# Kernel optimization log

Hardware: AMD Instinct MI355X
Metric: run time of the kernel (lower is better)

## Reference

```python
import jax, jax.numpy as jnp
import numpy as np

N_CLASSES = 19


def setup_inputs() -> dict:
    key = jax.random.key(0)
    k1, k2 = jax.random.split(key)
    embedding = jax.random.normal(k1, (4, 32, 128, 128), dtype=jnp.float32)
    label = jax.random.randint(k2, (4, 512, 512), 0, N_CLASSES, dtype=jnp.int64)
    return {"embedding": embedding, "label": label}


def _discriminative_loss(embedding, label, n_classes=N_CLASSES):
    N, H, W = label.shape
    C = embedding.shape[1]
    # bilinear upsample embedding to label resolution (F.upsample mode='bilinear')
    emb = jax.image.resize(embedding, (N, C, H, W), method="bilinear")
    HW = H * W
    emb = emb.reshape(N, C, HW).transpose(0, 2, 1)          # (N, HW, C)
    lab = label.reshape(N, HW)                               # (N, HW)

    onehot = jax.nn.one_hot(lab, n_classes, dtype=emb.dtype)  # (N, HW, K)
    count = onehot.sum(1)                                    # (N, K)
    mask = (count > 0).astype(emb.dtype)                     # (N, K)

    # per-class embedding sum and (biased, /(count+1)) mean
    cls_sum = jnp.einsum("npc,npk->nkc", emb, onehot)       # (N, K, C)
    cls_mean = cls_sum / (count[:, :, None] + 1.0)           # (N, K, C)

    # intra-class: per-pixel squared distance to own-class mean, mean over C
    mean_pp = jnp.take_along_axis(cls_mean, lab[:, :, None], axis=1)  # (N, HW, C)
    d2 = jnp.mean((emb - mean_pp) ** 2, axis=-1)             # (N, HW)
    intra_per_cls = jnp.einsum("np,npk->nk", d2, onehot) / (count + 1.0)  # (N, K)
    n_fg = mask[:, 1:].sum(1)                                # (N,)
    l2_intra = (intra_per_cls[:, 1:] * mask[:, 1:]).sum(1) / n_fg  # (N,)

    # inter-class: pairwise mean squared distance between class means
    diff = cls_mean[:, :, None, :] - cls_mean[:, None, :, :]  # (N, K, K, C)
    inter = jnp.mean(diff ** 2, axis=-1)                     # (N, K, K)
    inter = inter * mask[:, None, :] * mask[:, :, None]
    l2_inter = inter[:, 1:, 1:].reshape(N, -1).sum(1) / (n_fg * n_fg)  # (N,)

    return l2_intra - l2_inter


def reference(embedding, label):
    return _discriminative_loss(embedding, label)
```

## Files before the change

kernel.cpp:

```cpp
#include <hip/hip_runtime.h>

#define NIMG 4
#define NCLS 19
#define CCH  32
#define LH   128
#define LW   128
#define HH   512
#define WW   512
#define HWQ  (LH*LW)
#define HWP  (HH*WW)

#define TR 8
#define TC 8
#define NTX (LW/TC)
#define NTILE (256)
#define TCELLS (TR*TC)
#define RW 10
#define RING 100
#define NSLOT 608

__device__ __forceinline__ void taps(int v, int lim, int& i0, float& w0, float& w1) {
    int r = v & 3;
    int b = (v >> 2) + ((r < 2) ? -1 : 0);
    float f = 0.125f + 0.25f * (float)((r + 2) & 3);
    w0 = 1.f - f; w1 = f;
    if (b < 0)           { b = 0;       w0 = 1.f; w1 = 0.f; }
    else if (b >= lim)   { b = lim - 1; w0 = 0.f; w1 = 1.f; }
    i0 = b;
}

__device__ __forceinline__ float ring_fetch(const float* Gn, int i, int Y0, int X0) {
    int p = i / RING, r = i - p * RING;
    int gy = r / RW, gx = r - gy * RW;
    int yy = Y0 - 1 + gy; yy = yy < 0 ? 0 : (yy > LH - 1 ? LH - 1 : yy);
    int xx = X0 - 1 + gx; xx = xx < 0 ? 0 : (xx > LW - 1 ? LW - 1 : xx);
    return Gn[(size_t)p * HWQ + yy * LW + xx];
}

__global__ __launch_bounds__(256) void k_gram(const float* __restrict__ E,
        float* __restrict__ G) {
    int n = blockIdx.y, rp = blockIdx.x;
    int tid = threadIdx.x;
    int x = tid & 127, dy = tid >> 7;
    int y = rp * 2 + dy;
    int yn = (y < LH - 1) ? y + 1 : y;
    int xn = (x < LW - 1) ? x + 1 : x;
    bool fix = ((x & 63) == 63);
    const float* base = E + (size_t)n * CCH * HWQ;
    const float* Ea = base + y * LW + x;
    const float* Eb = base + yn * LW + x;
    const float* Eax = base + y * LW + xn;
    const float* Ebx = base + yn * LW + xn;
    float gs = 0.f, gh = 0.f, gv = 0.f, gda = 0.f;
#pragma unroll 8
    for (int c = 0; c < CCH; c++) {
        float a = Ea[(size_t)c * HWQ];
        float b = Eb[(size_t)c * HWQ];
        float ar = __shfl_down(a, 1);
        float br = __shfl_down(b, 1);
        if (fix) { ar = Eax[(size_t)c * HWQ]; br = Ebx[(size_t)c * HWQ]; }
        gs = fmaf(a, a, gs);
        gh = fmaf(a, ar, gh);
        gv = fmaf(a, b, gv);
        gda = fmaf(a, br, fmaf(ar, b, gda));
    }
    float* Gp = G + (size_t)n * 4 * HWQ + y * LW + x;
    Gp[0] = gs; Gp[HWQ] = gh; Gp[2 * HWQ] = gv; Gp[3 * HWQ] = gda;
}

__global__ __launch_bounds__(256, 4) void k_field(const float* __restrict__ E,
        const int* __restrict__ lab, const float* __restrict__ G,
        float* __restrict__ P_sum, float* __restrict__ P_cnt, float* __restrict__ P_S2) {
    int tile = blockIdx.x, n = blockIdx.y;
    int ty = tile >> 4, tx = tile & 15;
    int Y0 = ty * TR, X0 = tx * TC;
    __shared__ float A[TCELLS * NCLS];
    __shared__ float Gt[4 * RING];
    __shared__ float S2w[4 * NCLS];
    __shared__ float tmpc[NCLS * 8];
    __shared__ __align__(16) float cs_l[NSLOT];
    int tid = threadIdx.x;
    const int* ln = lab + (size_t)n * HWP;
    int h_lo = Y0 * 4 - 2;

    int hA, qA, hB = 0, qB = 0; bool vB;
    int4 LA, LB = make_int4(0, 0, 0, 0);
    {
        int hr = tid / RW, qi = tid - hr * RW;
        hA = h_lo + hr; qA = X0 - 1 + qi;
        int hc = hA < 0 ? 0 : (hA > HH - 1 ? HH - 1 : hA);
        int qc = qA < 0 ? 0 : (qA > LW - 1 ? LW - 1 : qA);
        LA = *(const int4*)(ln + hc * WW + (qc << 2));
    }
    vB = (tid < 360 - 256);
    if (vB) {
        int i = tid + 256;
        int hr = i / RW, qi = i - hr * RW;
        hB = h_lo + hr; qB = X0 - 1 + qi;
        int hc = hB < 0 ? 0 : (hB > HH - 1 ? HH - 1 : hB);
        int qc = qB < 0 ? 0 : (qB > LW - 1 ? LW - 1 : qB);
        LB = *(const int4*)(ln + hc * WW + (qc << 2));
    }
    int cc = tid >> 3, cy = tid & 7;
    const float* Er = E + ((size_t)n * CCH + cc) * HWQ + (Y0 + cy) * LW + X0;
    float4 ev0 = *(const float4*)Er;
    float4 ev1 = *(const float4*)(Er + 4);
    const float* Gn = G + (size_t)n * 4 * HWQ;
    float rv0 = ring_fetch(Gn, tid, Y0, X0);
    bool rB = (tid < 4 * RING - 256);
    float rv1 = rB ? ring_fetch(Gn, tid + 256, Y0, X0) : 0.f;

    for (int i = tid; i < TCELLS * NCLS; i += 256) A[i] = 0.f;
    if (tid < 4 * NCLS) S2w[tid] = 0.f;
    Gt[tid] = rv0;
    if (rB) Gt[tid + 256] = rv1;
    __syncthreads();

    const float* Gs_ = Gt, *Gh_ = Gt + RING, *Gv_ = Gt + 2 * RING, *Gda_ = Gt + 3 * RING;
    auto process = [&](int h, int q, int4 l4) {
        if (h < 0 || h >= HH || q < 0 || q >= LW) return;
        int y0; float wy0, wy1;
        taps(h, LH - 1, y0, wy0, wy1);
        int ry = y0 - Y0;
        bool r0 = (unsigned)ry < (unsigned)TR, r1 = (unsigned)(ry + 1) < (unsigned)TR;
        int rxm = q - 1 - X0, rx0 = q - X0, rxp = q + 1 - X0;
        bool bm = (unsigned)rxm < (unsigned)TC, b0 = (unsigned)rx0 < (unsigned)TC,
             bp = (unsigned)rxp < (unsigned)TC;
        bool fast = (q >= 1) && (q <= 126);
        bool owned = ((unsigned)(h - Y0 * 4) < 32u) && b0;
        if (fast) {
            if (r0) {
                int rb = (ry * TC) * NCLS;
                if (bm) { float* a = &A[rb + rxm * NCLS];
                    atomicAdd(a + l4.x, wy0 * 0.375f); atomicAdd(a + l4.y, wy0 * 0.125f); }
                if (b0) { float* a = &A[rb + rx0 * NCLS];
                    atomicAdd(a + l4.x, wy0 * 0.625f); atomicAdd(a + l4.y, wy0 * 0.875f);
                    atomicAdd(a + l4.z, wy0 * 0.875f); atomicAdd(a + l4.w, wy0 * 0.625f); }
                if (bp) { float* a = &A[rb + rxp * NCLS];
                    atomicAdd(a + l4.z, wy0 * 0.125f); atomicAdd(a + l4.w, wy0 * 0.375f); }
            }
            if (r1) {
                int rb = ((ry + 1) * TC) * NCLS;
                if (bm) { float* a = &A[rb + rxm * NCLS];
                    atomicAdd(a + l4.x, wy1 * 0.375f); atomicAdd(a + l4.y, wy1 * 0.125f); }
                if (b0) { float* a = &A[rb + rx0 * NCLS];
                    atomicAdd(a + l4.x, wy1 * 0.625f); atomicAdd(a + l4.y, wy1 * 0.875f);
                    atomicAdd(a + l4.z, wy1 * 0.875f); atomicAdd(a + l4.w, wy1 * 0.625f); }
                if (bp) { float* a = &A[rb + rxp * NCLS];
                    atomicAdd(a + l4.z, wy1 * 0.125f); atomicAdd(a + l4.w, wy1 * 0.375f); }
            }
            if (owned) {
                float u0 = wy0 * wy0, u1 = wy1 * wy1, u2t = 2.f * wy0 * wy1;
                int g00 = (y0 - Y0 + 1) * RW + rx0;
                float C0 = u0 * Gs_[g00]     + u1 * Gs_[g00 + RW]     + u2t * Gv_[g00];
                float C1 = u0 * Gs_[g00 + 1] + u1 * Gs_[g00 + RW + 1] + u2t * Gv_[g00 + 1];
                float C2 = u0 * Gs_[g00 + 2] + u1 * Gs_[g00 + RW + 2] + u2t * Gv_[g00 + 2];
                float D0 = 2.f * (u0 * Gh_[g00]     + u1 * Gh_[g00 + RW])     + u2t * Gda_[g00];
                float D1 = 2.f * (u0 * Gh_[g00 + 1] + u1 * Gh_[g00 + RW + 1]) + u2t * Gda_[g00 + 1];
                float d2a = fmaf(0.140625f, C0, fmaf(0.390625f, C1, 0.46875f * D0));
                float d2b = fmaf(0.015625f, C0, fmaf(0.765625f, C1, 0.21875f * D0));
                float d2c = fmaf(0.765625f, C1, fmaf(0.015625f, C2, 0.21875f * D1));
                float d2d = fmaf(0.390625f, C1, fmaf(0.140625f, C2, 0.46875f * D1));
                int wv = (tid >> 6) * NCLS;
                atomicAdd(&S2w[wv + l4.x], d2a); atomicAdd(&S2w[wv + l4.y], d2b);
                atomicAdd(&S2w[wv + l4.z], d2c); atomicAdd(&S2w[wv + l4.w], d2d);
            }
        } else {
            int Ls[4] = {l4.x, l4.y, l4.z, l4.w};
            float u0 = wy0 * wy0, u1 = wy1 * wy1, u2t = 2.f * wy0 * wy1;
            int gyr = y0 - Y0 + 1;
            int wv = (tid >> 6) * NCLS;
#pragma unroll
            for (int j = 0; j < 4; j++) {
                int w = (q << 2) + j;
                int x0; float wx0, wx1;
                taps(w, LW - 1, x0, wx0, wx1);
                int rxa = x0 - X0, rxb = rxa + 1;
                int L = Ls[j];
                if (r0) {
                    int rb = (ry * TC) * NCLS;
                    if ((unsigned)rxa < (unsigned)TC) atomicAdd(&A[rb + rxa * NCLS + L], wy0 * wx0);
                    if ((unsigned)rxb < (unsigned)TC) atomicAdd(&A[rb + rxb * NCLS + L], wy0 * wx1);
                }
                if (r1) {
                    int rb = ((ry + 1) * TC) * NCLS;
                    if ((unsigned)rxa < (unsigned)TC) atomicAdd(&A[rb + rxa * NCLS + L], wy1 * wx0);
                    if ((unsigned)rxb < (unsigned)TC) atomicAdd(&A[rb + rxb * NCLS + L], wy1 * wx1);
                }
                if (owned) {
                    int gg = gyr * RW + (x0 - X0 + 1);
                    float Ca = u0 * Gs_[gg]     + u1 * Gs_[gg + RW]     + u2t * Gv_[gg];
                    float Cb = u0 * Gs_[gg + 1] + u1 * Gs_[gg + RW + 1] + u2t * Gv_[gg + 1];
                    float Dd = 2.f * (u0 * Gh_[gg] + u1 * Gh_[gg + RW]) + u2t * Gda_[gg];
                    float d2 = wx0 * wx0 * Ca + wx1 * wx1 * Cb + 2.f * wx0 * wx1 * Dd;
                    atomicAdd(&S2w[wv + L], d2);
                }
            }
        }
    };
    process(hA, qA, LA);
    if (vB) process(hB, qB, LB);
    __syncthreads();

    {
        float ev[8] = {ev0.x, ev0.y, ev0.z, ev0.w, ev1.x, ev1.y, ev1.z, ev1.w};
        float acc[NCLS];
#pragma unroll
        for (int k = 0; k < NCLS; k++) acc[k] = 0.f;
#pragma unroll
        for (int cx = 0; cx < 8; cx++) {
            const float* Ar = &A[(cy * 8 + cx) * NCLS];
            float e = ev[cx];
#pragma unroll
            for (int k = 0; k < NCLS; k++) acc[k] = fmaf(Ar[k], e, acc[k]);
        }
#pragma unroll
        for (int k = 0; k < NCLS; k++) {
            acc[k] += __shfl_xor(acc[k], 1);
            acc[k] += __shfl_xor(acc[k], 2);
            acc[k] += __shfl_xor(acc[k], 4);
        }
        if (cy == 0) {
#pragma unroll
            for (int k = 0; k < NCLS; k++) cs_l[k * CCH + cc] = acc[k];
        }
    }
    if (tid < 8 * NCLS) {
        int g8 = tid / NCLS, k = tid - g8 * NCLS;
        float s = 0.f;
#pragma unroll
        for (int j = 0; j < 8; j++) s += A[(g8 * 8 + j) * NCLS + k];
        tmpc[k * 8 + g8] = s;
    }
    __syncthreads();

    float* Ps = P_sum + (size_t)(n * NTILE + tile) * NSLOT;
    if (tid < NSLOT / 4) ((float4*)Ps)[tid] = ((const float4*)cs_l)[tid];
    if (tid < NCLS) {
        float s = 0.f;
#pragma unroll
        for (int g8 = 0; g8 < 8; g8++) s += tmpc[tid * 8 + g8];
        P_cnt[(size_t)(n * NTILE + tile) * NCLS + tid] = s;
        P_S2[(size_t)(n * NTILE + tile) * NCLS + tid] =
            S2w[tid] + S2w[NCLS + tid] + S2w[2 * NCLS + tid] + S2w[3 * NCLS + tid];
    }
}

__global__ __launch_bounds__(256) void k_final(const float* __restrict__ P_sum,
        const float* __restrict__ P_cnt, const float* __restrict__ P_S2,
        float* __restrict__ out) {
    int n = blockIdx.x, tid = threadIdx.x;
    __shared__ double cs_d[NCLS * 33];
    __shared__ double m_d[NCLS * 33];
    __shared__ double cnt_d[NCLS], s2_d[NCLS];
    __shared__ double rk1[NCLS * 9], rk2[NCLS * 9];
    __shared__ double wpart[4];
    __shared__ double sIntra, sNfg;

    for (int i4 = tid; i4 < NSLOT / 4; i4 += 256) {
        const float4* p4 = (const float4*)(P_sum + (size_t)n * NTILE * NSLOT) + i4;
        double sx = 0.0, sy = 0.0, sz = 0.0, sw = 0.0;
#pragma unroll 4
        for (int t = 0; t < NTILE; t++) {
            float4 v = p4[(size_t)t * (NSLOT / 4)];
            sx += v.x; sy += v.y; sz += v.z; sw += v.w;
        }
        int idx = i4 * 4;
        int k = idx >> 5, c = idx & 31;
        cs_d[k * 33 + c] = sx; cs_d[k * 33 + c + 1] = sy;
        cs_d[k * 33 + c + 2] = sz; cs_d[k * 33 + c + 3] = sw;
    }
    if (tid < 8 * NCLS) {
        int k = tid >> 3, g = tid & 7;
        const float* p1 = P_cnt + ((size_t)n * NTILE + g * 32) * NCLS + k;
        const float* p2 = P_S2  + ((size_t)n * NTILE + g * 32) * NCLS + k;
        double s1 = 0.0, s2 = 0.0;
#pragma unroll 4
        for (int j = 0; j < 32; j++) { s1 += p1[j * NCLS]; s2 += p2[j * NCLS]; }
        rk1[k * 9 + g] = s1; rk2[k * 9 + g] = s2;
    }
    __syncthreads();
    if (tid < NCLS) {
        double s1 = 0.0, s2 = 0.0;
#pragma unroll
        for (int g = 0; g < 8; g++) { s1 += rk1[tid * 9 + g]; s2 += rk2[tid * 9 + g]; }
        cnt_d[tid] = s1; s2_d[tid] = s2;
    }
    __syncthreads();
    for (int idx = tid; idx < NSLOT; idx += 256) {
        int k = idx >> 5, c = idx & 31;
        m_d[k * 33 + c] = cs_d[k * 33 + c] / (cnt_d[k] + 1.0);
    }
    __syncthreads();
    double vi = 0.0, fg = 0.0;
    if (tid >= 1 && tid < NCLS && cnt_d[tid] > 0.0) {
        fg = 1.0;
        double dot = 0.0, mm = 0.0;
        for (int c = 0; c < CCH; c++) {
            double mv = m_d[tid * 33 + c];
            dot += mv * cs_d[tid * 33 + c];
            mm += mv * mv;
        }
        vi = (s2_d[tid] - 2.0 * dot + cnt_d[tid] * mm) * 0.03125 / (cnt_d[tid] + 1.0);
    }
    if (tid < 64) {
#pragma unroll
        for (int s_ = 32; s_ >= 1; s_ >>= 1) { vi += __shfl_xor(vi, s_); fg += __shfl_xor(fg, s_); }
        if (tid == 0) { sIntra = vi; sNfg = fg; }
    }
    double ve = 0.0;
    for (int t2 = tid; t2 < 324; t2 += 256) {
        int j = 1 + t2 / 18, k = 1 + t2 % 18;
        if (cnt_d[j] > 0.0 && cnt_d[k] > 0.0) {
            double s = 0.0;
            for (int c = 0; c < CCH; c++) {
                double d = m_d[j * 33 + c] - m_d[k * 33 + c];
                s += d * d;
            }
            ve += s * 0.03125;
        }
    }
#pragma unroll
    for (int s_ = 32; s_ >= 1; s_ >>= 1) ve += __shfl_xor(ve, s_);
    if ((tid & 63) == 0) wpart[tid >> 6] = ve;
    __syncthreads();
    if (tid == 0) {
        double inter = wpart[0] + wpart[1] + wpart[2] + wpart[3];
        out[n] = (float)(sIntra / sNfg - inter / (sNfg * sNfg));
    }
}

extern "C" void kernel_launch(void* const* d_in, const int* in_sizes, int n_in,
                              void* d_out, int out_size, void* d_ws, size_t ws_size,
                              hipStream_t stream) {
    const float* E = (const float*)d_in[0];
    const int* lab = (const int*)d_in[1];
    float* out = (float*)d_out;

    float* P_sum = (float*)d_ws;
    float* P_cnt = P_sum + (size_t)NIMG * NTILE * NSLOT;
    float* P_S2  = P_cnt + (size_t)NIMG * NTILE * NCLS;
    float* G     = P_S2  + (size_t)NIMG * NTILE * NCLS;

    k_gram <<<dim3(64, NIMG),    dim3(256), 0, stream>>>(E, G);
    k_field<<<dim3(NTILE, NIMG), dim3(256), 0, stream>>>(E, lab, G, P_sum, P_cnt, P_S2);
    k_final<<<dim3(NIMG),        dim3(256), 0, stream>>>(P_sum, P_cnt, P_S2, out);
}
```

Baseline: 141.4 us.

## Fuse Gram and S2 into banded kernel, fold final reduction into last block

```diff
diff --git a/kernel.cpp b/kernel.cpp
--- a/kernel.cpp
+++ b/kernel.cpp
@@ -12,12 +12,13 @@
 
 #define TR 8
 #define TC 8
-#define NTX (LW/TC)
-#define NTILE (256)
-#define TCELLS (TR*TC)
+#define NTX 16
+#define NTILE 256
+#define TCELLS 64
 #define RW 10
-#define RING 100
+#define HITEMS 360
 #define NSLOT 608
+#define NBAND 64
 
 __device__ __forceinline__ void taps(int v, int lim, int& i0, float& w0, float& w1) {
     int r = v & 3;
@@ -29,94 +30,156 @@
     i0 = b;
 }
 
-__device__ __forceinline__ float ring_fetch(const float* Gn, int i, int Y0, int X0) {
-    int p = i / RING, r = i - p * RING;
-    int gy = r / RW, gx = r - gy * RW;
-    int yy = Y0 - 1 + gy; yy = yy < 0 ? 0 : (yy > LH - 1 ? LH - 1 : yy);
-    int xx = X0 - 1 + gx; xx = xx < 0 ? 0 : (xx > LW - 1 ? LW - 1 : xx);
-    return Gn[(size_t)p * HWQ + yy * LW + xx];
+__global__ __launch_bounds__(512) void k_a(const float* __restrict__ E,
+        const int* __restrict__ lab, float* __restrict__ P_S2,
+        unsigned int* __restrict__ Cnt) {
+    int rp = blockIdx.x, n = blockIdx.y;
+    int tid = threadIdx.x;
+    int x = tid & 127, quarter = tid >> 7;
+    __shared__ float Gt[4 * 3 * 128];
+    __shared__ float S2w[32 * NCLS];
+    if (rp == 0 && n == 0 && tid < NIMG) Cnt[tid] = 0u;
+    for (int i = tid; i < 4 * 3 * 128; i += 512) Gt[i] = 0.f;
+    for (int i = tid; i < 32 * NCLS; i += 512) S2w[i] = 0.f;
+
+    int y0r = 2 * rp;
+    int yr[4];
+#pragma unroll
+    for (int j = 0; j < 4; j++) { int y = y0r + j; yr[j] = y > LH - 1 ? LH - 1 : y; }
+    int xn = x < LW - 1 ? x + 1 : LW - 1;
+    bool fix = ((x & 63) == 63);
+    const float* Eb = E + (size_t)(n * CCH + quarter * 8) * HWQ;
+    float gs0=0,gs1=0,gs2=0, gh0=0,gh1=0,gh2=0, gv0=0,gv1=0,gv2=0, gd0=0,gd1=0,gd2=0;
+    __syncthreads();
+#pragma unroll 4
+    for (int ci = 0; ci < 8; ci++) {
+        const float* Ec = Eb + (size_t)ci * HWQ;
+        float r0 = Ec[yr[0] * LW + x];
+        float r1 = Ec[yr[1] * LW + x];
+        float r2 = Ec[yr[2] * LW + x];
+        float r3 = Ec[yr[3] * LW + x];
+        float s0 = __shfl_down(r0, 1), s1 = __shfl_down(r1, 1);
+        float s2 = __shfl_down(r2, 1), s3 = __shfl_down(r3, 1);
+        if (fix) { s0 = Ec[yr[0] * LW + xn]; s1 = Ec[yr[1] * LW + xn];
+                   s2 = Ec[yr[2] * LW + xn]; s3 = Ec[yr[3] * LW + xn]; }
+        gs0 = fmaf(r0, r0, gs0); gh0 = fmaf(r0, s0, gh0);
+        gv0 = fmaf(r0, r1, gv0); gd0 = fmaf(r0, s1, fmaf(s0, r1, gd0));
+        gs1 = fmaf(r1, r1, gs1); gh1 = fmaf(r1, s1, gh1);
+        gv1 = fmaf(r1, r2, gv1); gd1 = fmaf(r1, s2, fmaf(s1, r2, gd1));
+        gs2 = fmaf(r2, r2, gs2); gh2 = fmaf(r2, s2, gh2);
+        gv2 = fmaf(r2, r3, gv2); gd2 = fmaf(r2, s3, fmaf(s2, r3, gd2));
+    }
+    atomicAdd(&Gt[0 * 384 + 0 * 128 + x], gs0);
+    atomicAdd(&Gt[0 * 384 + 1 * 128 + x], gs1);
+    atomicAdd(&Gt[0 * 384 + 2 * 128 + x], gs2);
+    atomicAdd(&Gt[1 * 384 + 0 * 128 + x], gh0);
+    atomicAdd(&Gt[1 * 384 + 1 * 128 + x], gh1);
+    atomicAdd(&Gt[1 * 384 + 2 * 128 + x], gh2);
+    atomicAdd(&Gt[2 * 384 + 0 * 128 + x], gv0);
+    atomicAdd(&Gt[2 * 384 + 1 * 128 + x], gv1);
+    atomicAdd(&Gt[2 * 384 + 2 * 128 + x], gv2);
+    atomicAdd(&Gt[3 * 384 + 0 * 128 + x], gd0);
+    atomicAdd(&Gt[3 * 384 + 1 * 128 + x], gd1);
+    atomicAdd(&Gt[3 * 384 + 2 * 128 + x], gd2);
+    __syncthreads();
+
+    const float* Gs_ = Gt, *Gh_ = Gt + 384, *Gv_ = Gt + 768, *Gda_ = Gt + 1152;
+    int h_start = (rp == 0) ? 0 : 8 * rp + 2;
+    int h_end = 8 * rp + 10; if (h_end > HH) h_end = HH;
+    int nItems = (h_end - h_start) * 128;
+    const int* ln = lab + (size_t)n * HWP;
+    for (int it = tid; it < nItems; it += 512) {
+        int h = h_start + (it >> 7), q = it & 127;
+        int y0; float wy0, wy1;
+        taps(h, LH - 1, y0, wy0, wy1);
+        int jj = y0 - y0r;
+        int4 l4 = *(const int4*)(ln + h * WW + (q << 2));
+        float u0 = wy0 * wy0, u1 = wy1 * wy1, u2t = 2.f * wy0 * wy1;
+        int b0 = jj * 128, b1 = b0 + 128;
+        int wv = (tid >> 4) * NCLS;
+        if (q >= 1 && q <= 126) {
+            int xm = q - 1;
+            float C0 = u0 * Gs_[b0 + xm]    + u1 * Gs_[b1 + xm]    + u2t * Gv_[b0 + xm];
+            float C1 = u0 * Gs_[b0 + q]     + u1 * Gs_[b1 + q]     + u2t * Gv_[b0 + q];
+            float C2 = u0 * Gs_[b0 + q + 1] + u1 * Gs_[b1 + q + 1] + u2t * Gv_[b0 + q + 1];
+            float D0 = 2.f * (u0 * Gh_[b0 + xm] + u1 * Gh_[b1 + xm]) + u2t * Gda_[b0 + xm];
+            float D1 = 2.f * (u0 * Gh_[b0 + q]  + u1 * Gh_[b1 + q])  + u2t * Gda_[b0 + q];
+            float d2a = fmaf(0.140625f, C0, fmaf(0.390625f, C1, 0.234375f * D0));
+            float d2b = fmaf(0.015625f, C0, fmaf(0.765625f, C1, 0.109375f * D0));
+            float d2c = fmaf(0.765625f, C1, fmaf(0.015625f, C2, 0.109375f * D1));
+            float d2d = fmaf(0.390625f, C1, fmaf(0.140625f, C2, 0.234375f * D1));
+            atomicAdd(&S2w[wv + l4.x], d2a); atomicAdd(&S2w[wv + l4.y], d2b);
+            atomicAdd(&S2w[wv + l4.z], d2c); atomicAdd(&S2w[wv + l4.w], d2d);
+        } else {
+            int Ls[4] = {l4.x, l4.y, l4.z, l4.w};
+#pragma unroll
+            for (int j2 = 0; j2 < 4; j2++) {
+                int w = (q << 2) + j2;
+                int x0; float wx0, wx1;
+                taps(w, LW - 1, x0, wx0, wx1);
+                float Ca = u0 * Gs_[b0 + x0]     + u1 * Gs_[b1 + x0]     + u2t * Gv_[b0 + x0];
+                float Cb = u0 * Gs_[b0 + x0 + 1] + u1 * Gs_[b1 + x0 + 1] + u2t * Gv_[b0 + x0 + 1];
+                float Dd = 2.f * (u0 * Gh_[b0 + x0] + u1 * Gh_[b1 + x0]) + u2t * Gda_[b0 + x0];
+                float d2 = wx0 * wx0 * Ca + wx1 * wx1 * Cb + wx0 * wx1 * Dd;
+                atomicAdd(&S2w[wv + Ls[j2]], d2);
+            }
+        }
+    }
+    __syncthreads();
+    if (tid < NCLS) {
+        float s = 0.f;
+#pragma unroll
+        for (int j = 0; j < 32; j++) s += S2w[j * NCLS + tid];
+        P_S2[(size_t)(n * NBAND + rp) * NCLS + tid] = s;
+    }
 }
 
-__global__ __launch_bounds__(256) void k_gram(const float* __restrict__ E,
-        float* __restrict__ G) {
-    int n = blockIdx.y, rp = blockIdx.x;
-    int tid = threadIdx.x;
-    int x = tid & 127, dy = tid >> 7;
-    int y = rp * 2 + dy;
-    int yn = (y < LH - 1) ? y + 1 : y;
-    int xn = (x < LW - 1) ? x + 1 : x;
-    bool fix = ((x & 63) == 63);
-    const float* base = E + (size_t)n * CCH * HWQ;
-    const float* Ea = base + y * LW + x;
-    const float* Eb = base + yn * LW + x;
-    const float* Eax = base + y * LW + xn;
-    const float* Ebx = base + yn * LW + xn;
-    float gs = 0.f, gh = 0.f, gv = 0.f, gda = 0.f;
-#pragma unroll 8
-    for (int c = 0; c < CCH; c++) {
-        float a = Ea[(size_t)c * HWQ];
-        float b = Eb[(size_t)c * HWQ];
-        float ar = __shfl_down(a, 1);
-        float br = __shfl_down(b, 1);
-        if (fix) { ar = Eax[(size_t)c * HWQ]; br = Ebx[(size_t)c * HWQ]; }
-        gs = fmaf(a, a, gs);
-        gh = fmaf(a, ar, gh);
-        gv = fmaf(a, b, gv);
-        gda = fmaf(a, br, fmaf(ar, b, gda));
-    }
-    float* Gp = G + (size_t)n * 4 * HWQ + y * LW + x;
-    Gp[0] = gs; Gp[HWQ] = gh; Gp[2 * HWQ] = gv; Gp[3 * HWQ] = gda;
-}
-
-__global__ __launch_bounds__(256, 4) void k_field(const float* __restrict__ E,
-        const int* __restrict__ lab, const float* __restrict__ G,
-        float* __restrict__ P_sum, float* __restrict__ P_cnt, float* __restrict__ P_S2) {
+__global__ __launch_bounds__(256, 6) void k_b(const float* __restrict__ E,
+        const int* __restrict__ lab, float* __restrict__ P_sum,
+        float* __restrict__ P_cnt, const float* __restrict__ P_S2,
+        unsigned int* __restrict__ Cnt, float* __restrict__ out) {
     int tile = blockIdx.x, n = blockIdx.y;
     int ty = tile >> 4, tx = tile & 15;
     int Y0 = ty * TR, X0 = tx * TC;
-    __shared__ float A[TCELLS * NCLS];
-    __shared__ float Gt[4 * RING];
-    __shared__ float S2w[4 * NCLS];
+    __shared__ float A[NCLS * TCELLS];
     __shared__ float tmpc[NCLS * 8];
     __shared__ __align__(16) float cs_l[NSLOT];
+    __shared__ unsigned int sdone;
+    __shared__ double cs_d[NCLS * 33];
+    __shared__ double m_d[NCLS * 33];
+    __shared__ double cnt_d[NCLS], s2_d[NCLS];
+    __shared__ double rk1[NCLS * 9];
+    __shared__ double rk2[NCLS * 5];
+    __shared__ double wpart[4];
+    __shared__ double sIntra, sNfg;
     int tid = threadIdx.x;
     const int* ln = lab + (size_t)n * HWP;
     int h_lo = Y0 * 4 - 2;
 
-    int hA, qA, hB = 0, qB = 0; bool vB;
-    int4 LA, LB = make_int4(0, 0, 0, 0);
+    int hA = h_lo + tid / RW, qA = X0 - 1 + tid % RW;
+    int4 LA;
     {
-        int hr = tid / RW, qi = tid - hr * RW;
-        hA = h_lo + hr; qA = X0 - 1 + qi;
         int hc = hA < 0 ? 0 : (hA > HH - 1 ? HH - 1 : hA);
         int qc = qA < 0 ? 0 : (qA > LW - 1 ? LW - 1 : qA);
         LA = *(const int4*)(ln + hc * WW + (qc << 2));
     }
-    vB = (tid < 360 - 256);
+    bool vB = tid < (HITEMS - 256);
+    int hB = 0, qB = 0; int4 LB = make_int4(0, 0, 0, 0);
     if (vB) {
         int i = tid + 256;
-        int hr = i / RW, qi = i - hr * RW;
-        hB = h_lo + hr; qB = X0 - 1 + qi;
+        hB = h_lo + i / RW; qB = X0 - 1 + i % RW;
         int hc = hB < 0 ? 0 : (hB > HH - 1 ? HH - 1 : hB);
         int qc = qB < 0 ? 0 : (qB > LW - 1 ? LW - 1 : qB);
         LB = *(const int4*)(ln + hc * WW + (qc << 2));
     }
     int cc = tid >> 3, cy = tid & 7;
-    const float* Er = E + ((size_t)n * CCH + cc) * HWQ + (Y0 + cy) * LW + X0;
-    float4 ev0 = *(const float4*)Er;
-    float4 ev1 = *(const float4*)(Er + 4);
-    const float* Gn = G + (size_t)n * 4 * HWQ;
-    float rv0 = ring_fetch(Gn, tid, Y0, X0);
-    bool rB = (tid < 4 * RING - 256);
-    float rv1 = rB ? ring_fetch(Gn, tid + 256, Y0, X0) : 0.f;
-
-    for (int i = tid; i < TCELLS * NCLS; i += 256) A[i] = 0.f;
-    if (tid < 4 * NCLS) S2w[tid] = 0.f;
-    Gt[tid] = rv0;
-    if (rB) Gt[tid + 256] = rv1;
-    __syncthreads();
-
-    const float* Gs_ = Gt, *Gh_ = Gt + RING, *Gv_ = Gt + 2 * RING, *Gda_ = Gt + 3 * RING;
+    const float* Er = E + (size_t)(n * CCH + cc) * HWQ + (Y0 + cy) * LW + X0;
+    float4 ev0 = ((const float4*)Er)[0];
+    float4 ev1 = ((const float4*)Er)[1];
+
+    for (int i = tid; i < NCLS * TCELLS; i += 256) A[i] = 0.f;
+    __syncthreads();
+
     auto process = [&](int h, int q, int4 l4) {
         if (h < 0 || h >= HH || q < 0 || q >= LW) return;
         int y0; float wy0, wy1;
@@ -126,50 +189,29 @@
         int rxm = q - 1 - X0, rx0 = q - X0, rxp = q + 1 - X0;
         bool bm = (unsigned)rxm < (unsigned)TC, b0 = (unsigned)rx0 < (unsigned)TC,
              bp = (unsigned)rxp < (unsigned)TC;
-        bool fast = (q >= 1) && (q <= 126);
-        bool owned = ((unsigned)(h - Y0 * 4) < 32u) && b0;
-        if (fast) {
+        if (q >= 1 && q <= 126) {
             if (r0) {
-                int rb = (ry * TC) * NCLS;
-                if (bm) { float* a = &A[rb + rxm * NCLS];
-                    atomicAdd(a + l4.x, wy0 * 0.375f); atomicAdd(a + l4.y, wy0 * 0.125f); }
-                if (b0) { float* a = &A[rb + rx0 * NCLS];
-                    atomicAdd(a + l4.x, wy0 * 0.625f); atomicAdd(a + l4.y, wy0 * 0.875f);
-                    atomicAdd(a + l4.z, wy0 * 0.875f); atomicAdd(a + l4.w, wy0 * 0.625f); }
-                if (bp) { float* a = &A[rb + rxp * NCLS];
-                    atomicAdd(a + l4.z, wy0 * 0.125f); atomicAdd(a + l4.w, wy0 * 0.375f); }
+                int rb = ry * TC;
+                if (bm) { float* a = &A[rb + rxm];
+                    atomicAdd(a + l4.x * TCELLS, wy0 * 0.375f); atomicAdd(a + l4.y * TCELLS, wy0 * 0.125f); }
+                if (b0) { float* a = &A[rb + rx0];
+                    atomicAdd(a + l4.x * TCELLS, wy0 * 0.625f); atomicAdd(a + l4.y * TCELLS, wy0 * 0.875f);
+                    atomicAdd(a + l4.z * TCELLS, wy0 * 0.875f); atomicAdd(a + l4.w * TCELLS, wy0 * 0.625f); }
+                if (bp) { float* a = &A[rb + rxp];
+                    atomicAdd(a + l4.z * TCELLS, wy0 * 0.125f); atomicAdd(a + l4.w * TCELLS, wy0 * 0.375f); }
             }
             if (r1) {
-                int rb = ((ry + 1) * TC) * NCLS;
-                if (bm) { float* a = &A[rb + rxm * NCLS];
-                    atomicAdd(a + l4.x, wy1 * 0.375f); atomicAdd(a + l4.y, wy1 * 0.125f); }
-                if (b0) { float* a = &A[rb + rx0 * NCLS];
-                    atomicAdd(a + l4.x, wy1 * 0.625f); atomicAdd(a + l4.y, wy1 * 0.875f);
-                    atomicAdd(a + l4.z, wy1 * 0.875f); atomicAdd(a + l4.w, wy1 * 0.625f); }
-                if (bp) { float* a = &A[rb + rxp * NCLS];
-                    atomicAdd(a + l4.z, wy1 * 0.125f); atomicAdd(a + l4.w, wy1 * 0.375f); }
-            }
-            if (owned) {
-                float u0 = wy0 * wy0, u1 = wy1 * wy1, u2t = 2.f * wy0 * wy1;
-                int g00 = (y0 - Y0 + 1) * RW + rx0;
-                float C0 = u0 * Gs_[g00]     + u1 * Gs_[g00 + RW]     + u2t * Gv_[g00];
-                float C1 = u0 * Gs_[g00 + 1] + u1 * Gs_[g00 + RW + 1] + u2t * Gv_[g00 + 1];
-                float C2 = u0 * Gs_[g00 + 2] + u1 * Gs_[g00 + RW + 2] + u2t * Gv_[g00 + 2];
-                float D0 = 2.f * (u0 * Gh_[g00]     + u1 * Gh_[g00 + RW])     + u2t * Gda_[g00];
-                float D1 = 2.f * (u0 * Gh_[g00 + 1] + u1 * Gh_[g00 + RW + 1]) + u2t * Gda_[g00 + 1];
-                float d2a = fmaf(0.140625f, C0, fmaf(0.390625f, C1, 0.46875f * D0));
-                float d2b = fmaf(0.015625f, C0, fmaf(0.765625f, C1, 0.21875f * D0));
-                float d2c = fmaf(0.765625f, C1, fmaf(0.015625f, C2, 0.21875f * D1));
-                float d2d = fmaf(0.390625f, C1, fmaf(0.140625f, C2, 0.46875f * D1));
-                int wv = (tid >> 6) * NCLS;
-                atomicAdd(&S2w[wv + l4.x], d2a); atomicAdd(&S2w[wv + l4.y], d2b);
-                atomicAdd(&S2w[wv + l4.z], d2c); atomicAdd(&S2w[wv + l4.w], d2d);
+                int rb = (ry + 1) * TC;
+                if (bm) { float* a = &A[rb + rxm];
+                    atomicAdd(a + l4.x * TCELLS, wy1 * 0.375f); atomicAdd(a + l4.y * TCELLS, wy1 * 0.125f); }
+                if (b0) { float* a = &A[rb + rx0];
+                    atomicAdd(a + l4.x * TCELLS, wy1 * 0.625f); atomicAdd(a + l4.y * TCELLS, wy1 * 0.875f);
+                    atomicAdd(a + l4.z * TCELLS, wy1 * 0.875f); atomicAdd(a + l4.w * TCELLS, wy1 * 0.625f); }
+                if (bp) { float* a = &A[rb + rxp];
+                    atomicAdd(a + l4.z * TCELLS, wy1 * 0.125f); atomicAdd(a + l4.w * TCELLS, wy1 * 0.375f); }
             }
         } else {
             int Ls[4] = {l4.x, l4.y, l4.z, l4.w};
-            float u0 = wy0 * wy0, u1 = wy1 * wy1, u2t = 2.f * wy0 * wy1;
-            int gyr = y0 - Y0 + 1;
-            int wv = (tid >> 6) * NCLS;
 #pragma unroll
             for (int j = 0; j < 4; j++) {
                 int w = (q << 2) + j;
@@ -178,22 +220,14 @@
                 int rxa = x0 - X0, rxb = rxa + 1;
                 int L = Ls[j];
                 if (r0) {
-                    int rb = (ry * TC) * NCLS;
-                    if ((unsigned)rxa < (unsigned)TC) atomicAdd(&A[rb + rxa * NCLS + L], wy0 * wx0);
-                    if ((unsigned)rxb < (unsigned)TC) atomicAdd(&A[rb + rxb * NCLS + L], wy0 * wx1);
+                    int rb = ry * TC;
+                    if ((unsigned)rxa < (unsigned)TC) atomicAdd(&A[L * TCELLS + rb + rxa], wy0 * wx0);
+                    if ((unsigned)rxb < (unsigned)TC) atomicAdd(&A[L * TCELLS + rb + rxb], wy0 * wx1);
                 }
                 if (r1) {
-                    int rb = ((ry + 1) * TC) * NCLS;
-                    if ((unsigned)rxa < (unsigned)TC) atomicAdd(&A[rb + rxa * NCLS + L], wy1 * wx0);
-                    if ((unsigned)rxb < (unsigned)TC) atomicAdd(&A[rb + rxb * NCLS + L], wy1 * wx1);
-                }
-                if (owned) {
-                    int gg = gyr * RW + (x0 - X0 + 1);
-                    float Ca = u0 * Gs_[gg]     + u1 * Gs_[gg + RW]     + u2t * Gv_[gg];
-                    float Cb = u0 * Gs_[gg + 1] + u1 * Gs_[gg + RW + 1] + u2t * Gv_[gg + 1];
-                    float Dd = 2.f * (u0 * Gh_[gg] + u1 * Gh_[gg + RW]) + u2t * Gda_[gg];
-                    float d2 = wx0 * wx0 * Ca + wx1 * wx1 * Cb + 2.f * wx0 * wx1 * Dd;
-                    atomicAdd(&S2w[wv + L], d2);
+                    int rb = (ry + 1) * TC;
+                    if ((unsigned)rxa < (unsigned)TC) atomicAdd(&A[L * TCELLS + rb + rxa], wy1 * wx0);
+                    if ((unsigned)rxb < (unsigned)TC) atomicAdd(&A[L * TCELLS + rb + rxb], wy1 * wx1);
                 }
             }
         }
@@ -203,16 +237,17 @@
     __syncthreads();
 
     {
-        float ev[8] = {ev0.x, ev0.y, ev0.z, ev0.w, ev1.x, ev1.y, ev1.z, ev1.w};
+        float ev_[8] = {ev0.x, ev0.y, ev0.z, ev0.w, ev1.x, ev1.y, ev1.z, ev1.w};
         float acc[NCLS];
 #pragma unroll
         for (int k = 0; k < NCLS; k++) acc[k] = 0.f;
+        int base = cy * TC;
 #pragma unroll
         for (int cx = 0; cx < 8; cx++) {
-            const float* Ar = &A[(cy * 8 + cx) * NCLS];
-            float e = ev[cx];
-#pragma unroll
-            for (int k = 0; k < NCLS; k++) acc[k] = fmaf(Ar[k], e, acc[k]);
+            float e = ev_[cx];
+            const float* Ac = &A[base + cx];
+#pragma unroll
+            for (int k = 0; k < NCLS; k++) acc[k] = fmaf(Ac[k * TCELLS], e, acc[k]);
         }
 #pragma unroll
         for (int k = 0; k < NCLS; k++) {
@@ -229,7 +264,7 @@
         int g8 = tid / NCLS, k = tid - g8 * NCLS;
         float s = 0.f;
 #pragma unroll
-        for (int j = 0; j < 8; j++) s += A[(g8 * 8 + j) * NCLS + k];
+        for (int j = 0; j < 8; j++) s += A[k * TCELLS + g8 * 8 + j];
         tmpc[k * 8 + g8] = s;
     }
     __syncthreads();
@@ -241,49 +276,50 @@
 #pragma unroll
         for (int g8 = 0; g8 < 8; g8++) s += tmpc[tid * 8 + g8];
         P_cnt[(size_t)(n * NTILE + tile) * NCLS + tid] = s;
-        P_S2[(size_t)(n * NTILE + tile) * NCLS + tid] =
-            S2w[tid] + S2w[NCLS + tid] + S2w[2 * NCLS + tid] + S2w[3 * NCLS + tid];
-    }
-}
-
-__global__ __launch_bounds__(256) void k_final(const float* __restrict__ P_sum,
-        const float* __restrict__ P_cnt, const float* __restrict__ P_S2,
-        float* __restrict__ out) {
-    int n = blockIdx.x, tid = threadIdx.x;
-    __shared__ double cs_d[NCLS * 33];
-    __shared__ double m_d[NCLS * 33];
-    __shared__ double cnt_d[NCLS], s2_d[NCLS];
-    __shared__ double rk1[NCLS * 9], rk2[NCLS * 9];
-    __shared__ double wpart[4];
-    __shared__ double sIntra, sNfg;
-
-    for (int i4 = tid; i4 < NSLOT / 4; i4 += 256) {
-        const float4* p4 = (const float4*)(P_sum + (size_t)n * NTILE * NSLOT) + i4;
-        double sx = 0.0, sy = 0.0, sz = 0.0, sw = 0.0;
+    }
+
+    __threadfence();
+    if (tid == 0) sdone = atomicAdd(&Cnt[n], 1u);
+    __syncthreads();
+    if (sdone != NTILE - 1) return;
+    __threadfence();
+
+    if (tid < NSLOT / 4) {
+        const float4* pb = (const float4*)(P_sum + (size_t)n * NTILE * NSLOT) + tid;
+        double ax = 0, ay = 0, az = 0, aw = 0, bx = 0, by = 0, bz = 0, bw = 0;
+        for (int t = 0; t < NTILE; t += 2) {
+            float4 v0 = pb[(size_t)t * (NSLOT / 4)];
+            float4 v1 = pb[(size_t)(t + 1) * (NSLOT / 4)];
+            ax += v0.x; ay += v0.y; az += v0.z; aw += v0.w;
+            bx += v1.x; by += v1.y; bz += v1.z; bw += v1.w;
+        }
+        int idx = tid * 4, k = idx >> 5, c = idx & 31;
+        cs_d[k * 33 + c] = ax + bx; cs_d[k * 33 + c + 1] = ay + by;
+        cs_d[k * 33 + c + 2] = az + bz; cs_d[k * 33 + c + 3] = aw + bw;
+    }
+    if (tid < 8 * NCLS) {
+        int g = tid / NCLS, k = tid - g * NCLS;
+        const float* p1 = P_cnt + ((size_t)n * NTILE + g * 32) * NCLS + k;
+        double s1 = 0.0;
 #pragma unroll 4
-        for (int t = 0; t < NTILE; t++) {
-            float4 v = p4[(size_t)t * (NSLOT / 4)];
-            sx += v.x; sy += v.y; sz += v.z; sw += v.w;
-        }
-        int idx = i4 * 4;
-        int k = idx >> 5, c = idx & 31;
-        cs_d[k * 33 + c] = sx; cs_d[k * 33 + c + 1] = sy;
-        cs_d[k * 33 + c + 2] = sz; cs_d[k * 33 + c + 3] = sw;
-    }
-    if (tid < 8 * NCLS) {
-        int k = tid >> 3, g = tid & 7;
-        const float* p1 = P_cnt + ((size_t)n * NTILE + g * 32) * NCLS + k;
-        const float* p2 = P_S2  + ((size_t)n * NTILE + g * 32) * NCLS + k;
-        double s1 = 0.0, s2 = 0.0;
+        for (int j = 0; j < 32; j++) s1 += p1[j * NCLS];
+        rk1[k * 9 + g] = s1;
+    }
+    if (tid < 4 * NCLS) {
+        int g = tid / NCLS, k = tid - g * NCLS;
+        const float* p2 = P_S2 + ((size_t)n * NBAND + g * 16) * NCLS + k;
+        double s2 = 0.0;
 #pragma unroll 4
-        for (int j = 0; j < 32; j++) { s1 += p1[j * NCLS]; s2 += p2[j * NCLS]; }
-        rk1[k * 9 + g] = s1; rk2[k * 9 + g] = s2;
+        for (int j = 0; j < 16; j++) s2 += p2[j * NCLS];
+        rk2[k * 5 + g] = s2;
     }
     __syncthreads();
     if (tid < NCLS) {
         double s1 = 0.0, s2 = 0.0;
 #pragma unroll
-        for (int g = 0; g < 8; g++) { s1 += rk1[tid * 9 + g]; s2 += rk2[tid * 9 + g]; }
+        for (int g = 0; g < 8; g++) s1 += rk1[tid * 9 + g];
+#pragma unroll
+        for (int g = 0; g < 4; g++) s2 += rk2[tid * 5 + g];
         cnt_d[tid] = s1; s2_d[tid] = s2;
     }
     __syncthreads();
@@ -340,9 +376,8 @@
     float* P_sum = (float*)d_ws;
     float* P_cnt = P_sum + (size_t)NIMG * NTILE * NSLOT;
     float* P_S2  = P_cnt + (size_t)NIMG * NTILE * NCLS;
-    float* G     = P_S2  + (size_t)NIMG * NTILE * NCLS;
-
-    k_gram <<<dim3(64, NIMG),    dim3(256), 0, stream>>>(E, G);
-    k_field<<<dim3(NTILE, NIMG), dim3(256), 0, stream>>>(E, lab, G, P_sum, P_cnt, P_S2);
-    k_final<<<dim3(NIMG),        dim3(256), 0, stream>>>(P_sum, P_cnt, P_S2, out);
+    unsigned int* Cnt = (unsigned int*)(P_S2 + (size_t)NIMG * NBAND * NCLS);
+
+    k_a<<<dim3(NBAND, NIMG), dim3(512), 0, stream>>>(E, lab, P_S2, Cnt);
+    k_b<<<dim3(NTILE, NIMG), dim3(256), 0, stream>>>(E, lab, P_sum, P_cnt, P_S2, Cnt, out);
 }
```

Result: slower. 254.5 us (+80.0%).
